# Kernel optimization log

Hardware: AMD Instinct MI355X
Metric: run time of the kernel (lower is better)

The kernel has to match this reference:

```python
import jax, jax.numpy as jnp
import numpy as np

D = 2048
H = 8
QK = D // 2
FF = 8192
CAP = 15.0
EPS = 1e-6

def _rmsnorm(x, w, eps=EPS):
    xf = x.astype(jnp.float32)
    var = jnp.mean(xf * xf, axis=-1, keepdims=True)
    return (w * xf * jax.lax.rsqrt(var + eps)).astype(x.dtype)

def _soft_cap(x, cap=CAP):
    return cap * jnp.tanh(x / cap)

def _mlstm_parallel(q, k, v, i_pre, f_pre):
    # q,k: [B,H,S,dqk]  v: [B,H,S,dv]  i_pre,f_pre: [B,H,S]
    B, Hn, S, dqk = q.shape
    logfg = jax.nn.log_sigmoid(f_pre)                      # [B,H,S]
    Fcum = jnp.cumsum(logfg, axis=-1)                      # [B,H,S]
    # D[t,s] = F_t - F_s + i_s for s<=t else -inf
    Dmat = Fcum[..., :, None] - Fcum[..., None, :] + i_pre[..., None, :]
    causal = jnp.tril(jnp.ones((S, S), dtype=bool))
    Dmat = jnp.where(causal, Dmat, -jnp.inf)
    m = jnp.max(Dmat, axis=-1, keepdims=True)              # [B,H,S,1]
    Smat = jnp.exp(Dmat - m)
    qk = jnp.einsum('bhsd,bhtd->bhst', q, k) / jnp.sqrt(jnp.float32(dqk))
    C = qk * Smat
    n = jnp.maximum(jnp.abs(jnp.sum(C, axis=-1, keepdims=True)), jnp.exp(-m))
    h = jnp.einsum('bhst,bhtd->bhsd', C / n, v)            # [B,H,S,dv]
    return h

def setup_inputs() -> dict:
    key = jax.random.key(0)
    ks = jax.random.split(key, 17)
    sc = 0.02
    inp = {
        'x': jax.random.normal(ks[0], (2, 2048, D), jnp.float32),
        'norm1_w': jnp.ones((D,), jnp.float32),
        'wq': jax.random.normal(ks[1], (D, QK), jnp.float32) * sc,
        'wk': jax.random.normal(ks[2], (D, QK), jnp.float32) * sc,
        'wv': jax.random.normal(ks[3], (D, D), jnp.float32) * sc,
        'w_ig': jax.random.normal(ks[4], (D, H), jnp.float32) * sc,
        'b_ig': jnp.zeros((H,), jnp.float32),
        'w_fg': jax.random.normal(ks[5], (D, H), jnp.float32) * sc,
        'b_fg': jnp.linspace(3.0, 6.0, H).astype(jnp.float32),
        'w_og': jax.random.normal(ks[6], (D, D), jnp.float32) * sc,
        'mh_w': jnp.ones((D,), jnp.float32),
        'w_out': jax.random.normal(ks[7], (D, D), jnp.float32) * sc,
        'norm2_w': jnp.ones((D,), jnp.float32),
        'w_gate': jax.random.normal(ks[8], (D, FF), jnp.float32) * sc,
        'w_up': jax.random.normal(ks[9], (D, FF), jnp.float32) * sc,
        'w_down': jax.random.normal(ks[10], (FF, D), jnp.float32) * sc,
    }
    return inp

def reference(x, norm1_w, wq, wk, wv, w_ig, b_ig, w_fg, b_fg, w_og, mh_w,
              w_out, norm2_w, w_gate, w_up, w_down):
    B, S, _ = x.shape
    dqk, dv = QK // H, D // H
    # --- xLSTM mixer sublayer (pre-norm) ---
    h_in = _rmsnorm(x, norm1_w)
    q = (h_in @ wq).reshape(B, S, H, dqk).transpose(0, 2, 1, 3)
    k = (h_in @ wk).reshape(B, S, H, dqk).transpose(0, 2, 1, 3)
    v = (h_in @ wv).reshape(B, S, H, dv).transpose(0, 2, 1, 3)
    o_pre = h_in @ w_og                                    # [B,S,D]
    i_pre = _soft_cap(h_in @ w_ig + b_ig).transpose(0, 2, 1)  # [B,H,S]
    f_pre = _soft_cap(h_in @ w_fg + b_fg).transpose(0, 2, 1)
    h = _mlstm_parallel(q, k, v, i_pre, f_pre)             # [B,H,S,dv]
    h = h.transpose(0, 2, 1, 3)                            # [B,S,H,dv]
    # per-head RMSNorm with weight reshaped [H,dv]
    hf = h.astype(jnp.float32)
    var = jnp.mean(hf * hf, axis=-1, keepdims=True)
    h_norm = hf * jax.lax.rsqrt(var + EPS) * mh_w.reshape(H, dv)
    h_norm = h_norm.reshape(B, S, D)
    h_out = jax.nn.sigmoid(o_pre) * h_norm
    x1 = x + h_out @ w_out
    # --- SwiGLU MLP sublayer (pre-norm) ---
    h2 = _rmsnorm(x1, norm2_w)
    mlp = (jax.nn.silu(h2 @ w_gate) * (h2 @ w_up)) @ w_down
    return x1 + mlp
```

## Files before the change

### kernel.cpp

```cpp
#include <hip/hip_runtime.h>
#include <math.h>

typedef __bf16 bf16_t;
typedef __bf16 bf16x8 __attribute__((ext_vector_type(8)));
typedef float  floatx4 __attribute__((ext_vector_type(4)));

#define D_MODEL 2048
#define NH      8
#define DQK     128
#define DV      256
#define SEQ     2048
#define MROWS   4096
#define QKVO_N  6144
#define FF      8192


__device__ __forceinline__ void glds16(const void* g, void* l) {
  __builtin_amdgcn_global_load_lds(
      (const __attribute__((address_space(1))) void*)g,
      (__attribute__((address_space(3))) void*)l, 16, 0, 0);
}

__global__ __launch_bounds__(256) void transpose_bf16_kernel(
    const float* __restrict__ in, bf16_t* __restrict__ out, int K, int N) {
  __shared__ float tile[64][65];
  int n0 = blockIdx.x * 64, k0 = blockIdx.y * 64;
  int tx = threadIdx.x & 63, tg = threadIdx.x >> 6;
#pragma unroll
  for (int i = tg; i < 64; i += 4)
    tile[i][tx] = in[(size_t)(k0 + i) * N + n0 + tx];
  __syncthreads();
#pragma unroll
  for (int i = tg; i < 64; i += 4)
    out[(size_t)(n0 + i) * K + k0 + tx] = (bf16_t)tile[tx][i];
}

__global__ __launch_bounds__(256) void vtrans_kernel(
    const bf16_t* __restrict__ qkvo, bf16_t* __restrict__ vt) {
  __shared__ bf16_t tile[64 * 64];
  int s0 = blockIdx.x * 64;
  int d0 = blockIdx.y * 64;
  int bh = blockIdx.z;
  int b = bh >> 3, h = bh & 7;
  int tid = threadIdx.x;
  int r = tid >> 3, c8 = tid & 7;
#pragma unroll
  for (int u = 0; u < 2; ++u) {
    int rr = r + u * 32;
    bf16x8 v = *(const bf16x8*)&qkvo[(size_t)(b * SEQ + s0 + rr) * QKVO_N +
                                     2048 + h * DV + d0 + c8 * 8];
#pragma unroll
    for (int e = 0; e < 8; ++e) {
      int d = c8 * 8 + e;
      tile[d * 64 + (rr ^ ((e ^ c8) * 8))] = v[e];
    }
  }
  __syncthreads();
#pragma unroll
  for (int u = 0; u < 2; ++u) {
    int rr = r + u * 32;
    int cc = (c8 ^ (rr & 7) ^ ((rr >> 3) & 7)) * 8;
    bf16x8 v = *(const bf16x8*)&tile[rr * 64 + cc];
    *(bf16x8*)&vt[((size_t)bh * DV + d0 + rr) * SEQ + s0 + c8 * 8] = v;
  }
}

template<bool GATES>
__global__ __launch_bounds__(256) void rmsnorm_kernel(
    const float* __restrict__ xin, const float* __restrict__ w,
    bf16_t* __restrict__ out,
    const float* __restrict__ w_ig, const float* __restrict__ b_ig,
    const float* __restrict__ w_fg, const float* __restrict__ b_fg,
    float* __restrict__ gate_pre) {
  int row = blockIdx.x, tid = threadIdx.x;
  int lane = tid & 63, wvi = tid >> 6;
  const float* xr = xin + (size_t)row * D_MODEL;
  floatx4 v0 = *(const floatx4*)&xr[tid * 8];
  floatx4 v1 = *(const floatx4*)&xr[tid * 8 + 4];
  float ss = 0.f;
#pragma unroll
  for (int e = 0; e < 4; ++e) ss += v0[e] * v0[e] + v1[e] * v1[e];
#pragma unroll
  for (int off = 32; off > 0; off >>= 1) ss += __shfl_down(ss, off, 64);
  __shared__ float red[4];
  if (lane == 0) red[wvi] = ss;
  __syncthreads();
  float scale = rsqrtf((red[0] + red[1] + red[2] + red[3]) * (1.0f / D_MODEL) + 1e-6f);
  floatx4 w0 = *(const floatx4*)&w[tid * 8];
  floatx4 w1 = *(const floatx4*)&w[tid * 8 + 4];
  float h[8];
#pragma unroll
  for (int e = 0; e < 4; ++e) { h[e] = v0[e] * w0[e] * scale; h[4 + e] = v1[e] * w1[e] * scale; }
  bf16x8 ob;
#pragma unroll
  for (int e = 0; e < 8; ++e) ob[e] = (bf16_t)h[e];
  *(bf16x8*)&out[(size_t)row * D_MODEL + tid * 8] = ob;
  if constexpr (GATES) {
    float pg[16];
#pragma unroll
    for (int j = 0; j < 16; ++j) pg[j] = 0.f;
    int c0 = tid * 8;
#pragma unroll
    for (int e = 0; e < 8; ++e) {
      const float* wi = w_ig + (size_t)(c0 + e) * NH;
      const float* wf = w_fg + (size_t)(c0 + e) * NH;
#pragma unroll
      for (int j = 0; j < 8; ++j) { pg[j] += h[e] * wi[j]; pg[8 + j] += h[e] * wf[j]; }
    }
#pragma unroll
    for (int j = 0; j < 16; ++j) {
#pragma unroll
      for (int off = 32; off > 0; off >>= 1) pg[j] += __shfl_down(pg[j], off, 64);
    }
    __shared__ float redg[4][16];
    if (lane == 0) {
#pragma unroll
      for (int j = 0; j < 16; ++j) redg[wvi][j] = pg[j];
    }
    __syncthreads();
    if (tid < 16) {
      float t = redg[0][tid] + redg[1][tid] + redg[2][tid] + redg[3][tid];
      float bias = (tid < 8) ? b_ig[tid] : b_fg[tid - 8];
      gate_pre[(size_t)row * 16 + tid] = 15.0f * tanhf((t + bias) * (1.0f / 15.0f));
    }
  }
}

__global__ __launch_bounds__(64) void gate_scan_kernel(
    const float* __restrict__ gate_pre, float* __restrict__ ftb,
    float* __restrict__ Gb, float* __restrict__ mb) {
  int bh = blockIdx.x;
  int b = bh >> 3, h = bh & 7;
  int lane = threadIdx.x;
  const int CH = SEQ / 64;
  float lf[CH], iv[CH];
  float ls = 0.f;
#pragma unroll
  for (int c = 0; c < CH; ++c) {
    int s = lane * CH + c;
    const float* gp = &gate_pre[(size_t)(b * SEQ + s) * 16];
    float fg = gp[8 + h];
    iv[c] = gp[h];
    float v = fminf(fg, 0.f) - log1pf(expf(-fabsf(fg)));
    lf[c] = v; ls += v;
  }
  float xs = ls;
#pragma unroll
  for (int off = 1; off < 64; off <<= 1) {
    float y = __shfl_up(xs, off, 64);
    if (lane >= off) xs += y;
  }
  float F0 = xs - ls;
  float Fc = F0, Gv[CH], Fcs[CH], lmax = -3.0e38f;
#pragma unroll
  for (int c = 0; c < CH; ++c) {
    Fc += lf[c]; Fcs[c] = Fc;
    float g = iv[c] - Fc; Gv[c] = g;
    lmax = fmaxf(lmax, g);
  }
  float mx = lmax;
#pragma unroll
  for (int off = 1; off < 64; off <<= 1) {
    float y = __shfl_up(mx, off, 64);
    if (lane >= off) mx = fmaxf(mx, y);
  }
  float prev = __shfl_up(mx, 1, 64);
  if (lane == 0) prev = -3.0e38f;
  float run = prev;
  size_t base = (size_t)bh * SEQ + lane * CH;
  const float LOG_ISQ = -2.42601515f;
#pragma unroll
  for (int c = 0; c < CH; ++c) {
    run = fmaxf(run, Gv[c]);
    ftb[base + c] = -run + LOG_ISQ;
    Gb[base + c]  = Gv[c];
    mb[base + c]  = Fcs[c] + run;
  }
}

template<int EPI>
__global__ __launch_bounds__(256) void gemm_kernel(
    const bf16_t* __restrict__ A, const bf16_t* __restrict__ Bt,
    int N, int K,
    float* __restrict__ Cf, const float* __restrict__ Xres,
    bf16_t* __restrict__ Cb, const bf16_t* __restrict__ Gg) {
  __shared__ bf16_t sA[128 * 32];
  __shared__ bf16_t sB[128 * 32];
  int tid = threadIdx.x;
  int wv = tid >> 6, lane = tid & 63;
  int m0 = blockIdx.y * 128, n0 = blockIdx.x * 128;
  int lrow = lane >> 2, lseg = lane & 3;
  const bf16_t* gA = A + (size_t)(m0 + wv * 16 + lrow) * K + lseg * 8;
  const bf16_t* gB = Bt + (size_t)(n0 + wv * 16 + lrow) * K + lseg * 8;
  bf16_t* lA0 = &sA[(wv * 16) * 32];
  bf16_t* lA1 = &sA[(wv * 16 + 64) * 32];
  bf16_t* lB0 = &sB[(wv * 16) * 32];
  bf16_t* lB1 = &sB[(wv * 16 + 64) * 32];
  size_t skip = (size_t)64 * K;

  int wm = wv & 1, wn = wv >> 1;
  int r16 = lane & 15, q4 = lane >> 4;
  floatx4 acc[4][4];
#pragma unroll
  for (int i = 0; i < 4; ++i)
#pragma unroll
    for (int j = 0; j < 4; ++j) {
      acc[i][j][0] = 0.f; acc[i][j][1] = 0.f; acc[i][j][2] = 0.f; acc[i][j][3] = 0.f;
    }

  int niter = K >> 5;
  for (int kt = 0; kt < niter; ++kt) {
    const bf16_t* pA = gA + kt * 32;
    const bf16_t* pB = gB + kt * 32;
    glds16(pA, lA0);
    glds16(pA + skip, lA1);
    glds16(pB, lB0);
    glds16(pB + skip, lB1);
    __syncthreads();
    bf16x8 af[4], bfr[4];
#pragma unroll
    for (int i = 0; i < 4; ++i)
      af[i] = *(const bf16x8*)&sA[(wm * 64 + i * 16 + r16) * 32 + q4 * 8];
#pragma unroll
    for (int j = 0; j < 4; ++j)
      bfr[j] = *(const bf16x8*)&sB[(wn * 64 + j * 16 + r16) * 32 + q4 * 8];
#pragma unroll
    for (int i = 0; i < 4; ++i)
#pragma unroll
      for (int j = 0; j < 4; ++j)
        acc[i][j] = __builtin_amdgcn_mfma_f32_16x16x32_bf16(af[i], bfr[j], acc[i][j], 0, 0, 0);
    __syncthreads();
  }
#pragma unroll
  for (int i = 0; i < 4; ++i) {
#pragma unroll
    for (int r = 0; r < 4; ++r) {
      int grow = m0 + wm * 64 + i * 16 + q4 * 4 + r;
      size_t rb = (size_t)grow * N;
#pragma unroll
      for (int j = 0; j < 4; ++j) {
        int gcol = n0 + wn * 64 + j * 16 + r16;
        float v = acc[i][j][r];
        if constexpr (EPI == 0) {
          Cb[rb + gcol] = (bf16_t)v;
        } else if constexpr (EPI == 1) {
          Cf[rb + gcol] = Xres[rb + gcol] + v;
        } else if constexpr (EPI == 2) {
          float g = (float)Gg[rb + gcol];
          Cb[rb + gcol] = (bf16_t)((g / (1.f + expf(-g))) * v);
        } else {
          Cf[rb + gcol] += v;
        }
      }
    }
  }
}

__global__ __launch_bounds__(256) void attn_kernel(
    const bf16_t* __restrict__ qkvo, const bf16_t* __restrict__ vt,
    const float* __restrict__ ftb, const float* __restrict__ Gb,
    const float* __restrict__ mb, const float* __restrict__ mh_w,
    bf16_t* __restrict__ h_out) {
  constexpr int PS = 72;
  __shared__ bf16_t sP[32 * PS];
  __shared__ float sRS[32][2];
  __shared__ float sMS[32][4];
  __shared__ float sInvN[32];
  __shared__ float sSc[32];
  int p = blockIdx.x, bh = blockIdx.y;
  int b = bh >> 3, h = bh & 7;
  int tid = threadIdx.x;
  int wv = tid >> 6, lane = tid & 63;
  int r16 = lane & 15, q4 = lane >> 4;
  int mf = wv & 1, nh = wv >> 1;
  int dvb = wv * 64;
  size_t bh_off = (size_t)bh * SEQ;

  float mw[4];
#pragma unroll
  for (int nf = 0; nf < 4; ++nf) mw[nf] = mh_w[h * DV + dvb + nf * 16 + r16];

  for (int half = 0; half < 2; ++half) {
    int tt = half ? (63 - p) : p;
    int t0 = tt * 32;
    __syncthreads();
    bf16x8 qf[4];
    {
      const bf16_t* qrow =
          qkvo + (size_t)(b * SEQ + t0 + mf * 16 + r16) * QKVO_N + h * DQK + q4 * 8;
#pragma unroll
      for (int kt = 0; kt < 4; ++kt) qf[kt] = *(const bf16x8*)(qrow + kt * 32);
    }
    float ft[4];
#pragma unroll
    for (int r = 0; r < 4; ++r) ft[r] = ftb[bh_off + t0 + mf * 16 + q4 * 4 + r];

    floatx4 Of[2][4];
#pragma unroll
    for (int i = 0; i < 2; ++i)
#pragma unroll
      for (int j = 0; j < 4; ++j) Of[i][j] = (floatx4){0.f, 0.f, 0.f, 0.f};
    float rs[4] = {0.f, 0.f, 0.f, 0.f};

    int nst = (tt >> 1) + 1;
    const bf16_t* kp =
        qkvo + (size_t)(b * SEQ + nh * 32 + r16) * QKVO_N + 1024 + h * DQK + q4 * 8;
    const bf16_t* vp = vt + ((size_t)bh * DV + dvb + r16) * SEQ + q4 * 8;
    for (int st = 0; st < nst; ++st) {
      int s0 = st * 64;
      floatx4 sc[2] = {{0.f, 0.f, 0.f, 0.f}, {0.f, 0.f, 0.f, 0.f}};
#pragma unroll
      for (int nf = 0; nf < 2; ++nf) {
        const bf16_t* kpn = kp + (size_t)(s0 + nf * 16) * QKVO_N;
#pragma unroll
        for (int kt = 0; kt < 4; ++kt) {
          bf16x8 kf = *(const bf16x8*)(kpn + kt * 32);
          sc[nf] = __builtin_amdgcn_mfma_f32_16x16x32_bf16(qf[kt], kf, sc[nf], 0, 0, 0);
        }
      }
      bool diag = (st == nst - 1);
#pragma unroll
      for (int nf = 0; nf < 2; ++nf) {
        int scol = s0 + nh * 32 + nf * 16 + r16;
        float g = Gb[bh_off + scol];
#pragma unroll
        for (int r = 0; r < 4; ++r) {
          int trow = t0 + mf * 16 + q4 * 4 + r;
          float w = __expf(ft[r] + g) * sc[nf][r];
          if (diag && scol > trow) w = 0.f;
          rs[r] += w;
          sP[(mf * 16 + q4 * 4 + r) * PS + nh * 32 + nf * 16 + r16] = (bf16_t)w;
        }
      }
      __syncthreads();
      bf16x8 pa[2][2];
#pragma unroll
      for (int i = 0; i < 2; ++i)
#pragma unroll
        for (int kt = 0; kt < 2; ++kt)
          pa[i][kt] = *(const bf16x8*)&sP[(i * 16 + r16) * PS + kt * 32 + q4 * 8];
#pragma unroll
      for (int nf = 0; nf < 4; ++nf) {
        const bf16_t* vpn = vp + (size_t)(nf * 16) * SEQ + s0;
#pragma unroll
        for (int kt = 0; kt < 2; ++kt) {
          bf16x8 vf = *(const bf16x8*)(vpn + kt * 32);
#pragma unroll
          for (int i = 0; i < 2; ++i)
            Of[i][nf] = __builtin_amdgcn_mfma_f32_16x16x32_bf16(pa[i][kt], vf, Of[i][nf], 0, 0, 0);
        }
      }
      __syncthreads();
    }
#pragma unroll
    for (int r = 0; r < 4; ++r) {
#pragma unroll
      for (int off = 1; off < 16; off <<= 1) rs[r] += __shfl_xor(rs[r], off, 16);
    }
    if (r16 == 0) {
#pragma unroll
      for (int r = 0; r < 4; ++r) sRS[mf * 16 + q4 * 4 + r][nh] = rs[r];
    }
    __syncthreads();
    if (tid < 32) {
      float s = sRS[tid][0] + sRS[tid][1];
      sInvN[tid] = 1.0f / fmaxf(fabsf(s), __expf(-mb[bh_off + t0 + tid]));
    }
    __syncthreads();
    float msq[2][4] = {{0.f, 0.f, 0.f, 0.f}, {0.f, 0.f, 0.f, 0.f}};
#pragma unroll
    for (int i = 0; i < 2; ++i) {
#pragma unroll
      for (int r = 0; r < 4; ++r) {
        float inv = sInvN[i * 16 + q4 * 4 + r];
#pragma unroll
        for (int nf = 0; nf < 4; ++nf) {
          float v = Of[i][nf][r] * inv;
          Of[i][nf][r] = v;
          msq[i][r] += v * v;
        }
      }
    }
#pragma unroll
    for (int i = 0; i < 2; ++i)
#pragma unroll
      for (int r = 0; r < 4; ++r) {
#pragma unroll
        for (int off = 1; off < 16; off <<= 1) msq[i][r] += __shfl_xor(msq[i][r], off, 16);
      }
    if (r16 == 0) {
#pragma unroll
      for (int i = 0; i < 2; ++i)
#pragma unroll
        for (int r = 0; r < 4; ++r) sMS[i * 16 + q4 * 4 + r][wv] = msq[i][r];
    }
    __syncthreads();
    if (tid < 32) {
      float s = sMS[tid][0] + sMS[tid][1] + sMS[tid][2] + sMS[tid][3];
      sSc[tid] = rsqrtf(s * (1.0f / DV) + 1e-6f);
    }
    __syncthreads();
#pragma unroll
    for (int i = 0; i < 2; ++i) {
#pragma unroll
      for (int r = 0; r < 4; ++r) {
        int trow = t0 + i * 16 + q4 * 4 + r;
        size_t gr = (size_t)(b * SEQ + trow);
        float scl = sSc[i * 16 + q4 * 4 + r];
#pragma unroll
        for (int nf = 0; nf < 4; ++nf) {
          int col = h * DV + dvb + nf * 16 + r16;
          float op = (float)qkvo[gr * QKVO_N + 4096 + col];
          float sig = 1.0f / (1.0f + __expf(-op));
          h_out[gr * D_MODEL + col] = (bf16_t)(Of[i][nf][r] * scl * mw[nf] * sig);
        }
      }
    }
  }
}


extern "C" void kernel_launch(void* const* d_in, const int* in_sizes, int n_in,
                              void* d_out, int out_size, void* d_ws, size_t ws_size,
                              hipStream_t stream) {
  const float* x      = (const float*)d_in[0];
  const float* n1w    = (const float*)d_in[1];
  const float* wq     = (const float*)d_in[2];
  const float* wk     = (const float*)d_in[3];
  const float* wvp    = (const float*)d_in[4];
  const float* w_ig   = (const float*)d_in[5];
  const float* b_ig   = (const float*)d_in[6];
  const float* w_fg   = (const float*)d_in[7];
  const float* b_fg   = (const float*)d_in[8];
  const float* w_og   = (const float*)d_in[9];
  const float* mh_w   = (const float*)d_in[10];
  const float* w_out  = (const float*)d_in[11];
  const float* n2w    = (const float*)d_in[12];
  const float* w_gate = (const float*)d_in[13];
  const float* w_up   = (const float*)d_in[14];
  const float* w_down = (const float*)d_in[15];
  float* out = (float*)d_out;
  (void)in_sizes; (void)n_in; (void)out_size; (void)ws_size;

  char* base = (char*)d_ws;
  size_t off = 0;
  auto alloc = [&](size_t bytes) -> void* {
    void* pp = base + off;
    off += (bytes + 255) & ~(size_t)255;
    return pp;
  };
  bf16_t* wT_qkvo = (bf16_t*)alloc((size_t)QKVO_N * 2048 * 2);
  bf16_t* wT_out  = (bf16_t*)alloc((size_t)2048 * 2048 * 2);
  bf16_t* wT_gate = (bf16_t*)alloc((size_t)FF * 2048 * 2);
  bf16_t* wT_up   = (bf16_t*)alloc((size_t)FF * 2048 * 2);
  bf16_t* wT_down = (bf16_t*)alloc((size_t)2048 * FF * 2);
  bf16_t* h_in    = (bf16_t*)alloc((size_t)MROWS * 2048 * 2);
  float*  gate_pre= (float*)alloc((size_t)MROWS * 16 * 4);
  float*  ftb     = (float*)alloc((size_t)16 * SEQ * 4);
  float*  Gbuf    = (float*)alloc((size_t)16 * SEQ * 4);
  float*  mbuf    = (float*)alloc((size_t)16 * SEQ * 4);
  bf16_t* qkvo    = (bf16_t*)alloc((size_t)MROWS * QKVO_N * 2);
  bf16_t* h_out   = (bf16_t*)alloc((size_t)MROWS * 2048 * 2);
  bf16_t* gbuf    = (bf16_t*)alloc((size_t)MROWS * FF * 2);
  bf16_t* tbuf    = qkvo;
  bf16_t* vtbuf   = h_in;

  dim3 blk(256);
  transpose_bf16_kernel<<<dim3(16, 32), blk, 0, stream>>>(wq, wT_qkvo, 2048, 1024);
  transpose_bf16_kernel<<<dim3(16, 32), blk, 0, stream>>>(wk, wT_qkvo + (size_t)1024 * 2048, 2048, 1024);
  transpose_bf16_kernel<<<dim3(32, 32), blk, 0, stream>>>(wvp, wT_qkvo + (size_t)2048 * 2048, 2048, 2048);
  transpose_bf16_kernel<<<dim3(32, 32), blk, 0, stream>>>(w_og, wT_qkvo + (size_t)4096 * 2048, 2048, 2048);
  transpose_bf16_kernel<<<dim3(32, 32), blk, 0, stream>>>(w_out, wT_out, 2048, 2048);
  transpose_bf16_kernel<<<dim3(128, 32), blk, 0, stream>>>(w_gate, wT_gate, 2048, FF);
  transpose_bf16_kernel<<<dim3(128, 32), blk, 0, stream>>>(w_up, wT_up, 2048, FF);
  transpose_bf16_kernel<<<dim3(32, 128), blk, 0, stream>>>(w_down, wT_down, FF, 2048);

  rmsnorm_kernel<true><<<MROWS, blk, 0, stream>>>(x, n1w, h_in, w_ig, b_ig, w_fg, b_fg, gate_pre);
  gate_scan_kernel<<<16, 64, 0, stream>>>(gate_pre, ftb, Gbuf, mbuf);

  gemm_kernel<0><<<dim3(QKVO_N / 128, 32), blk, 0, stream>>>(
      h_in, wT_qkvo, QKVO_N, 2048, nullptr, nullptr, qkvo, nullptr);

  vtrans_kernel<<<dim3(32, 4, 16), blk, 0, stream>>>(qkvo, vtbuf);
  attn_kernel<<<dim3(32, 16), blk, 0, stream>>>(qkvo, vtbuf, ftb, Gbuf, mbuf, mh_w, h_out);

  gemm_kernel<1><<<dim3(16, 32), blk, 0, stream>>>(
      h_out, wT_out, 2048, 2048, out, x, nullptr, nullptr);

  rmsnorm_kernel<false><<<MROWS, blk, 0, stream>>>(out, n2w, h_in,
      nullptr, nullptr, nullptr, nullptr, nullptr);

  gemm_kernel<0><<<dim3(FF / 128, 32), blk, 0, stream>>>(
      h_in, wT_gate, FF, 2048, nullptr, nullptr, gbuf, nullptr);
  gemm_kernel<2><<<dim3(FF / 128, 32), blk, 0, stream>>>(
      h_in, wT_up, FF, 2048, nullptr, nullptr, tbuf, gbuf);
  gemm_kernel<3><<<dim3(16, 32), blk, 0, stream>>>(
      tbuf, wT_down, 2048, FF, out, nullptr, nullptr, nullptr);
}
```

Measured before the change: 1.405 ms.

## Fuse gate and up GEMMs via interleaved weights with direct-global-load MFMA kernel

Gate and up weight transposes now write into one buffer, interleaved in 16-row groups. A single GEMM then produces gate and up tiles side by side and applies SiLU(g)*u in registers. This removes the separate gate GEMM, the bf16 gate intermediate buffer and its reload, and shares reads of the A operand. The new GEMM loads fragments straight from global memory with no LDS staging. That gives up shared-memory reuse and may be bound by global memory latency.

```diff
diff --git a/kernel.cpp b/kernel.cpp
--- a/kernel.cpp
+++ b/kernel.cpp
@@ -21,8 +21,9 @@
       (__attribute__((address_space(3))) void*)l, 16, 0, 0);
 }
 
+template<int ILV>
 __global__ __launch_bounds__(256) void transpose_bf16_kernel(
-    const float* __restrict__ in, bf16_t* __restrict__ out, int K, int N) {
+    const float* __restrict__ in, bf16_t* __restrict__ out, int K, int N, int ioff) {
   __shared__ float tile[64][65];
   int n0 = blockIdx.x * 64, k0 = blockIdx.y * 64;
   int tx = threadIdx.x & 63, tg = threadIdx.x >> 6;
@@ -31,8 +32,11 @@
     tile[i][tx] = in[(size_t)(k0 + i) * N + n0 + tx];
   __syncthreads();
 #pragma unroll
-  for (int i = tg; i < 64; i += 4)
-    out[(size_t)(n0 + i) * K + k0 + tx] = (bf16_t)tile[tx][i];
+  for (int i = tg; i < 64; i += 4) {
+    int n = n0 + i;
+    size_t orow = ILV ? (size_t)(((n >> 4) << 5) + (n & 15) + ioff) : (size_t)n;
+    out[orow * K + k0 + tx] = (bf16_t)tile[tx][i];
+  }
 }
 
 __global__ __launch_bounds__(256) void vtrans_kernel(
@@ -183,7 +187,7 @@
     const bf16_t* __restrict__ A, const bf16_t* __restrict__ Bt,
     int N, int K,
     float* __restrict__ Cf, const float* __restrict__ Xres,
-    bf16_t* __restrict__ Cb, const bf16_t* __restrict__ Gg) {
+    bf16_t* __restrict__ Cb) {
   __shared__ bf16_t sA[128 * 32];
   __shared__ bf16_t sB[128 * 32];
   int tid = threadIdx.x;
@@ -245,11 +249,70 @@
           Cb[rb + gcol] = (bf16_t)v;
         } else if constexpr (EPI == 1) {
           Cf[rb + gcol] = Xres[rb + gcol] + v;
-        } else if constexpr (EPI == 2) {
-          float g = (float)Gg[rb + gcol];
-          Cb[rb + gcol] = (bf16_t)((g / (1.f + expf(-g))) * v);
         } else {
           Cf[rb + gcol] += v;
+        }
+      }
+    }
+  }
+}
+
+template<int EPI>
+__global__ __launch_bounds__(256) void gemm_dg_kernel(
+    const bf16_t* __restrict__ A, const bf16_t* __restrict__ Bt,
+    int N, int K,
+    float* __restrict__ Cf, bf16_t* __restrict__ Cb) {
+  int tid = threadIdx.x;
+  int wv = tid >> 6, lane = tid & 63;
+  int r16 = lane & 15, q4 = lane >> 4;
+  int wm = wv & 1, wn = wv >> 1;
+  int m0 = blockIdx.y * 128, n0 = blockIdx.x * 128;
+  const bf16_t* pA = A + (size_t)(m0 + wm * 64 + r16) * K + q4 * 8;
+  const bf16_t* pB = Bt + (size_t)(n0 + wn * 64 + r16) * K + q4 * 8;
+  size_t rstep = (size_t)16 * K;
+
+  floatx4 acc[4][4];
+#pragma unroll
+  for (int i = 0; i < 4; ++i)
+#pragma unroll
+    for (int j = 0; j < 4; ++j) {
+      acc[i][j][0] = 0.f; acc[i][j][1] = 0.f; acc[i][j][2] = 0.f; acc[i][j][3] = 0.f;
+    }
+
+#pragma unroll 2
+  for (int k = 0; k < K; k += 32) {
+    bf16x8 af[4], bfr[4];
+#pragma unroll
+    for (int i = 0; i < 4; ++i) af[i] = *(const bf16x8*)(pA + i * rstep + k);
+#pragma unroll
+    for (int j = 0; j < 4; ++j) bfr[j] = *(const bf16x8*)(pB + j * rstep + k);
+#pragma unroll
+    for (int i = 0; i < 4; ++i)
+#pragma unroll
+      for (int j = 0; j < 4; ++j)
+        acc[i][j] = __builtin_amdgcn_mfma_f32_16x16x32_bf16(af[i], bfr[j], acc[i][j], 0, 0, 0);
+  }
+
+#pragma unroll
+  for (int i = 0; i < 4; ++i) {
+#pragma unroll
+    for (int r = 0; r < 4; ++r) {
+      int grow = m0 + wm * 64 + i * 16 + q4 * 4 + r;
+      if constexpr (EPI == 5) {
+        size_t rb = (size_t)grow * (N >> 1);
+#pragma unroll
+        for (int jj = 0; jj < 2; ++jj) {
+          float g = acc[i][2 * jj][r];
+          float u = acc[i][2 * jj + 1][r];
+          int c = (blockIdx.x * 4 + wn * 2 + jj) * 16 + r16;
+          Cb[rb + c] = (bf16_t)((g / (1.f + __expf(-g))) * u);
+        }
+      } else {
+        size_t rb = (size_t)grow * N;
+#pragma unroll
+        for (int j = 0; j < 4; ++j) {
+          int gcol = n0 + wn * 64 + j * 16 + r16;
+          Cf[rb + gcol] += acc[i][j][r];
         }
       }
     }
@@ -451,8 +514,7 @@
   };
   bf16_t* wT_qkvo = (bf16_t*)alloc((size_t)QKVO_N * 2048 * 2);
   bf16_t* wT_out  = (bf16_t*)alloc((size_t)2048 * 2048 * 2);
-  bf16_t* wT_gate = (bf16_t*)alloc((size_t)FF * 2048 * 2);
-  bf16_t* wT_up   = (bf16_t*)alloc((size_t)FF * 2048 * 2);
+  bf16_t* wT_gu   = (bf16_t*)alloc((size_t)2 * FF * 2048 * 2);
   bf16_t* wT_down = (bf16_t*)alloc((size_t)2048 * FF * 2);
   bf16_t* h_in    = (bf16_t*)alloc((size_t)MROWS * 2048 * 2);
   float*  gate_pre= (float*)alloc((size_t)MROWS * 16 * 4);
@@ -461,39 +523,36 @@
   float*  mbuf    = (float*)alloc((size_t)16 * SEQ * 4);
   bf16_t* qkvo    = (bf16_t*)alloc((size_t)MROWS * QKVO_N * 2);
   bf16_t* h_out   = (bf16_t*)alloc((size_t)MROWS * 2048 * 2);
-  bf16_t* gbuf    = (bf16_t*)alloc((size_t)MROWS * FF * 2);
   bf16_t* tbuf    = qkvo;
   bf16_t* vtbuf   = h_in;
 
   dim3 blk(256);
-  transpose_bf16_kernel<<<dim3(16, 32), blk, 0, stream>>>(wq, wT_qkvo, 2048, 1024);
-  transpose_bf16_kernel<<<dim3(16, 32), blk, 0, stream>>>(wk, wT_qkvo + (size_t)1024 * 2048, 2048, 1024);
-  transpose_bf16_kernel<<<dim3(32, 32), blk, 0, stream>>>(wvp, wT_qkvo + (size_t)2048 * 2048, 2048, 2048);
-  transpose_bf16_kernel<<<dim3(32, 32), blk, 0, stream>>>(w_og, wT_qkvo + (size_t)4096 * 2048, 2048, 2048);
-  transpose_bf16_kernel<<<dim3(32, 32), blk, 0, stream>>>(w_out, wT_out, 2048, 2048);
-  transpose_bf16_kernel<<<dim3(128, 32), blk, 0, stream>>>(w_gate, wT_gate, 2048, FF);
-  transpose_bf16_kernel<<<dim3(128, 32), blk, 0, stream>>>(w_up, wT_up, 2048, FF);
-  transpose_bf16_kernel<<<dim3(32, 128), blk, 0, stream>>>(w_down, wT_down, FF, 2048);
+  transpose_bf16_kernel<0><<<dim3(16, 32), blk, 0, stream>>>(wq, wT_qkvo, 2048, 1024, 0);
+  transpose_bf16_kernel<0><<<dim3(16, 32), blk, 0, stream>>>(wk, wT_qkvo + (size_t)1024 * 2048, 2048, 1024, 0);
+  transpose_bf16_kernel<0><<<dim3(32, 32), blk, 0, stream>>>(wvp, wT_qkvo + (size_t)2048 * 2048, 2048, 2048, 0);
+  transpose_bf16_kernel<0><<<dim3(32, 32), blk, 0, stream>>>(w_og, wT_qkvo + (size_t)4096 * 2048, 2048, 2048, 0);
+  transpose_bf16_kernel<0><<<dim3(32, 32), blk, 0, stream>>>(w_out, wT_out, 2048, 2048, 0);
+  transpose_bf16_kernel<1><<<dim3(128, 32), blk, 0, stream>>>(w_gate, wT_gu, 2048, FF, 0);
+  transpose_bf16_kernel<1><<<dim3(128, 32), blk, 0, stream>>>(w_up, wT_gu, 2048, FF, 16);
+  transpose_bf16_kernel<0><<<dim3(32, 128), blk, 0, stream>>>(w_down, wT_down, FF, 2048, 0);
 
   rmsnorm_kernel<true><<<MROWS, blk, 0, stream>>>(x, n1w, h_in, w_ig, b_ig, w_fg, b_fg, gate_pre);
   gate_scan_kernel<<<16, 64, 0, stream>>>(gate_pre, ftb, Gbuf, mbuf);
 
   gemm_kernel<0><<<dim3(QKVO_N / 128, 32), blk, 0, stream>>>(
-      h_in, wT_qkvo, QKVO_N, 2048, nullptr, nullptr, qkvo, nullptr);
+      h_in, wT_qkvo, QKVO_N, 2048, nullptr, nullptr, qkvo);
 
   vtrans_kernel<<<dim3(32, 4, 16), blk, 0, stream>>>(qkvo, vtbuf);
   attn_kernel<<<dim3(32, 16), blk, 0, stream>>>(qkvo, vtbuf, ftb, Gbuf, mbuf, mh_w, h_out);
 
   gemm_kernel<1><<<dim3(16, 32), blk, 0, stream>>>(
-      h_out, wT_out, 2048, 2048, out, x, nullptr, nullptr);
+      h_out, wT_out, 2048, 2048, out, x, nullptr);
 
   rmsnorm_kernel<false><<<MROWS, blk, 0, stream>>>(out, n2w, h_in,
       nullptr, nullptr, nullptr, nullptr, nullptr);
 
-  gemm_kernel<0><<<dim3(FF / 128, 32), blk, 0, stream>>>(
-      h_in, wT_gate, FF, 2048, nullptr, nullptr, gbuf, nullptr);
-  gemm_kernel<2><<<dim3(FF / 128, 32), blk, 0, stream>>>(
-      h_in, wT_up, FF, 2048, nullptr, nullptr, tbuf, gbuf);
+  gemm_dg_kernel<5><<<dim3(2 * FF / 128, 32), blk, 0, stream>>>(
+      h_in, wT_gu, 2 * FF, 2048, nullptr, tbuf);
   gemm_kernel<3><<<dim3(16, 32), blk, 0, stream>>>(
-      tbuf, wT_down, 2048, FF, out, nullptr, nullptr, nullptr);
-}
+      tbuf, wT_down, 2048, FF, out, nullptr, nullptr);
+}
```

After: 1.926 ms. 1.37x slower.
